# Kernel optimization log

Hardware: AMD Instinct MI355X
Metric: run time of the kernel (lower is better)

The kernel has to match this reference:

```python
import jax, jax.numpy as jnp
import numpy as np

DIM = 768
HID = 1536
EPS = 1e-12
SCALE = float(np.sqrt(DIM))


def _layernorm(x, gamma, beta):
    mu = jnp.mean(x, axis=-1, keepdims=True)
    var = jnp.mean(jnp.square(x - mu), axis=-1, keepdims=True)
    return (x - mu) * jax.lax.rsqrt(var + EPS) * gamma + beta


def setup_inputs() -> dict:
    key = jax.random.key(0)
    ks = jax.random.split(key, 16)
    s = 1.0 / np.sqrt(DIM)
    sh = 1.0 / np.sqrt(HID)
    x = jax.random.normal(ks[0], (8, 2048, DIM), dtype=jnp.float32)
    return {
        "x": x,
        "Wq": jax.random.uniform(ks[1], (DIM, DIM), jnp.float32, -s, s),
        "bq": jax.random.uniform(ks[2], (DIM,), jnp.float32, -s, s),
        "Wk": jax.random.uniform(ks[3], (DIM, DIM), jnp.float32, -s, s),
        "bk": jax.random.uniform(ks[4], (DIM,), jnp.float32, -s, s),
        "Wv": jax.random.uniform(ks[5], (DIM, DIM), jnp.float32, -s, s),
        "bv": jax.random.uniform(ks[6], (DIM,), jnp.float32, -s, s),
        "Wp": jax.random.uniform(ks[7], (DIM, DIM), jnp.float32, -s, s),
        "bp": jax.random.uniform(ks[8], (DIM,), jnp.float32, -s, s),
        "g1": jnp.ones((DIM,), jnp.float32),
        "be1": jnp.zeros((DIM,), jnp.float32),
        "W1": jax.random.uniform(ks[9], (HID, DIM), jnp.float32, -s, s),
        "b1": jax.random.uniform(ks[10], (HID,), jnp.float32, -s, s),
        "W2": jax.random.uniform(ks[11], (DIM, HID), jnp.float32, -sh, sh),
        "b2": jax.random.uniform(ks[12], (DIM,), jnp.float32, -sh, sh),
        "g2": jnp.ones((DIM,), jnp.float32),
        "be2": jnp.zeros((DIM,), jnp.float32),
    }


def reference(x, Wq, bq, Wk, bk, Wv, bv, Wp, bp, g1, be1, W1, b1, W2, b2, g2, be2):
    # NOTE: original code does NOT split into heads; single full-dim bmm attention.
    Q = jnp.einsum("bsd,ed->bse", x, Wq) + bq  # [B,S,D]
    K = jnp.einsum("bsd,ed->bse", x, Wk) + bk
    V = jnp.einsum("bsd,ed->bse", x, Wv) + bv
    alpha = jnp.einsum("bqd,bkd->bqk", Q, K) / SCALE  # [B,S,S]
    alpha = jax.nn.softmax(alpha, axis=-1)
    attn = jnp.einsum("bqk,bkd->bqd", alpha, V)
    attn = jnp.einsum("bsd,ed->bse", attn, Wp) + bp  # linear_proj
    h = _layernorm(x + attn, g1, be1)
    mlp = jax.nn.gelu(jnp.einsum("bsd,hd->bsh", h, W1) + b1, approximate=False)
    mlp = jnp.einsum("bsh,dh->bsd", mlp, W2) + b2
    return _layernorm(h + mlp, g2, be2)
```

## Files before the change

### kernel.cpp

```cpp
#include <hip/hip_runtime.h>
#include <math.h>

#define D_MODEL 768
#define D_HID   1536
#define N_BATCH 8
#define SEQLEN  2048
#define NROWS   (N_BATCH*SEQLEN)

typedef unsigned short u16;
typedef unsigned char  u8;
typedef __attribute__((ext_vector_type(8))) short bfrag;
typedef __attribute__((ext_vector_type(4))) float facc;

__device__ __forceinline__ u16 f2bf(float f) {
  unsigned u = __float_as_uint(f);
  u += 0x7fffu + ((u >> 16) & 1u);
  return (u16)(u >> 16);
}
__device__ __forceinline__ float bf2f(u16 u) {
  return __uint_as_float((unsigned)u << 16);
}
__device__ __forceinline__ u8 f2fp8(float f) {
  return (u8)(__builtin_amdgcn_cvt_pk_fp8_f32(f, f, 0, 0) & 0xff);
}

__device__ __forceinline__ void async16(const void* g, void* l) {
  __builtin_amdgcn_global_load_lds((const __attribute__((address_space(1))) void*)g,
                                   (__attribute__((address_space(3))) void*)l,
                                   16, 0, 0);
}
__device__ __forceinline__ void wg_barrier() {
  asm volatile("" ::: "memory");
  __builtin_amdgcn_s_barrier();
  asm volatile("" ::: "memory");
}
#define VMCNT(n) asm volatile("s_waitcnt vmcnt(" #n ")" ::: "memory")

__global__ __launch_bounds__(256) void cvt_all(
    const float* __restrict__ x,  const float* __restrict__ Wq,
    const float* __restrict__ Wk, const float* __restrict__ Wv,
    const float* __restrict__ Wp, const float* __restrict__ W1,
    const float* __restrict__ W2, const float* __restrict__ bq,
    const float* __restrict__ bk, const float* __restrict__ bv,
    u16* __restrict__ XB, u16* __restrict__ WQKV, u16* __restrict__ WPB,
    u16* __restrict__ W1B, u16* __restrict__ W2B, float* __restrict__ BQKV,
    float* __restrict__ LSUM) {
  long i = (long)blockIdx.x * 256 + threadIdx.x;
  const float* src; u16* dst; long off;
  if      (i < 3145728) { src = x;  dst = XB;             off = i; }
  else if (i < 3293184) { src = Wq; dst = WQKV;           off = i - 3145728; }
  else if (i < 3440640) { src = Wk; dst = WQKV + 589824;  off = i - 3293184; }
  else if (i < 3588096) { src = Wv; dst = WQKV + 1179648; off = i - 3440640; }
  else if (i < 3735552) { src = Wp; dst = WPB;            off = i - 3588096; }
  else if (i < 4030464) { src = W1; dst = W1B;            off = i - 3735552; }
  else if (i < 4325376) { src = W2; dst = W2B;            off = i - 4030464; }
  else if (i < 4325952) {
    long j = i - 4325376;
    const float* s = (j < 192) ? bq : (j < 384) ? bk : bv;
    long o = (j < 192) ? j : (j < 384) ? j - 192 : j - 384;
    ((float4*)BQKV)[j] = ((const float4*)s)[o];
    return;
  } else if (i < 4330048) {
    float4 zz = {0.f, 0.f, 0.f, 0.f};
    ((float4*)LSUM)[i - 4325952] = zz;
    return;
  } else return;
  float4 v = ((const float4*)src)[off];
  ushort4 o4;
  o4.x = f2bf(v.x); o4.y = f2bf(v.y); o4.z = f2bf(v.z); o4.w = f2bf(v.w);
  *reinterpret_cast<ushort4*>(dst + off * 4) = o4;
}

enum { EPI_EXP = 1, EPI_DIV = 2, EPI_GELU = 4, EPI_QKV = 5, EPI_RES = 6 };

template<int EPI>
__global__ __launch_bounds__(512, 4)
void gemm_bt(const u16* __restrict__ Aall, const u16* __restrict__ Ball,
             void* __restrict__ Cout,
             int M, int N, int K,
             long sA, long sB, long sC,
             const float* __restrict__ bias,
             const u16* __restrict__ resid,
             float* __restrict__ lsum,
             float scale)
{
  __shared__ __align__(16) char smem[73728];
  const int z = blockIdx.z;
  const u16* A = Aall + (long)z * sA;
  const u16* B = Ball + (long)z * sB;
  const int bm = blockIdx.x, bn = blockIdx.y;
  const int tid = (int)threadIdx.x;
  const int lane = tid & 63, wv = tid >> 6;
  const int wr = wv >> 2, wc = wv & 3;

  facc acc[4][4] = {};

  const int srow = tid >> 2;
  const int sc = (((tid & 3) ^ (srow & 3)) << 3);
  const u16* Abase = A + (long)(bm * 128) * K;
  const u16* Bbase = B + (long)(bn * 256) * K;
  const int fr = lane & 15, g0 = lane >> 4;
  const int nt = K >> 5;

  auto STAGE = [&](int t, int b) {
    char* Asb = smem + b * 24576;
    char* Bsb = Asb + 8192;
    const long k0 = (long)t << 5;
    async16(Abase + (long)srow * K + k0 + sc, Asb + tid * 16);
    async16(Bbase + (long)srow * K + k0 + sc, Bsb + tid * 16);
    async16(Bbase + (long)(128 + srow) * K + k0 + sc, Bsb + 8192 + tid * 16);
  };

  STAGE(0, 0); STAGE(1, 1);
  int rb_ = 0, sb_ = 2;
  for (int t = 0; t < nt; ++t) {
    if (t < nt - 1) { VMCNT(3); } else { VMCNT(0); }
    wg_barrier();
    if (t + 2 < nt) STAGE(t + 2, sb_);
    const u16* As = (const u16*)(smem + rb_ * 24576);
    const u16* Bs = As + 4096;
    bfrag af[4], bf[4];
#pragma unroll
    for (int i = 0; i < 4; ++i) {
      const int r = wr * 64 + i * 16 + fr;
      af[i] = *(const bfrag*)(As + r * 32 + ((g0 ^ (r & 3)) << 3));
    }
#pragma unroll
    for (int j = 0; j < 4; ++j) {
      const int r = wc * 64 + j * 16 + fr;
      bf[j] = *(const bfrag*)(Bs + r * 32 + ((g0 ^ (r & 3)) << 3));
    }
    __builtin_amdgcn_s_setprio(1);
#pragma unroll
    for (int i = 0; i < 4; ++i)
#pragma unroll
      for (int j = 0; j < 4; ++j)
        acc[i][j] = __builtin_amdgcn_mfma_f32_16x16x32_bf16(af[i], bf[j], acc[i][j], 0, 0, 0);
    __builtin_amdgcn_s_setprio(0);
    rb_ = (rb_ == 2) ? 0 : rb_ + 1;
    sb_ = (sb_ == 2) ? 0 : sb_ + 1;
  }
  wg_barrier();

  const int rb = bm * 128 + wr * 64;
  const int cb = bn * 256 + wc * 64;
  const int quad = lane >> 4;

  if constexpr (EPI == EPI_QKV) {
    const int c64 = bn * 4 + wc;
    const int which = c64 / 12;
    float bj[4];
#pragma unroll
    for (int j = 0; j < 4; ++j) bj[j] = bias[cb + j * 16 + fr];
    if (which == 2) {
      u8* VT_ = (u8*)resid;
      const int zb = rb >> 11;
      const int seqb = (rb & 2047) + quad * 4;
      const int dimb = (c64 - 24) * 64;
#pragma unroll
      for (int i = 0; i < 4; ++i) {
#pragma unroll
        for (int j = 0; j < 4; ++j) {
          const int dim = dimb + j * 16 + fr;
          unsigned v01 = __builtin_amdgcn_cvt_pk_fp8_f32(acc[i][j][0] + bj[j],
                                                         acc[i][j][1] + bj[j], 0, 0);
          unsigned v23 = __builtin_amdgcn_cvt_pk_fp8_f32(acc[i][j][2] + bj[j],
                                                         acc[i][j][3] + bj[j], 0, 0);
          unsigned w = (v01 & 0xffffu) | (v23 << 16);
          *reinterpret_cast<unsigned*>(VT_ + (long)zb * D_MODEL * SEQLEN +
                                       (long)dim * SEQLEN + seqb + i * 16) = w;
        }
      }
      return;
    }
    u8* ep8 = (u8*)(smem + wv * 8192);
    u8* Cg = (u8*)Cout + (long)which * NROWS * D_MODEL;
    const int cbo = (c64 - which * 12) * 64;
#pragma unroll
    for (int i = 0; i < 4; ++i)
#pragma unroll
      for (int r = 0; r < 4; ++r) {
        const int lrow = i * 16 + quad * 4 + r;
#pragma unroll
        for (int j = 0; j < 4; ++j)
          ep8[lrow * 64 + j * 16 + fr] = f2fp8(acc[i][j][r] + bj[j]);
      }
#pragma unroll
    for (int it = 0; it < 4; ++it) {
      const int lr = it * 16 + (lane >> 2);
      const int ch = (lane & 3) << 4;
      int4 d = *(const int4*)(ep8 + lr * 64 + ch);
      *reinterpret_cast<int4*>(Cg + (long)(rb + lr) * D_MODEL + cbo + ch) = d;
    }
  } else {
    u16* ep16 = (u16*)(smem + wv * 8192);
    u16* Cg = (u16*)Cout + (long)z * sC;
    float bj[4];
#pragma unroll
    for (int j = 0; j < 4; ++j) bj[j] = bias[cb + j * 16 + fr];
#pragma unroll
    for (int i = 0; i < 4; ++i) {
#pragma unroll
      for (int r = 0; r < 4; ++r) {
        const int lrow = i * 16 + quad * 4 + r;
#pragma unroll
        for (int j = 0; j < 4; ++j) {
          float t = acc[i][j][r] + bj[j];
          float y = 0.7978845608f * (t + 0.044715f * t * t * t);
          float e = __expf(-2.f * fabsf(y));
          float th = (1.f - e) / (1.f + e);
          th = (y < 0.f) ? -th : th;
          ep16[lrow * 64 + j * 16 + fr] = f2bf(0.5f * t * (1.f + th));
        }
      }
    }
#pragma unroll
    for (int it = 0; it < 8; ++it) {
      const int lr = it * 8 + (lane >> 3);
      const int ch = (lane & 7) << 3;
      int4 d = *(const int4*)(ep16 + lr * 64 + ch);
      *reinterpret_cast<int4*>(Cg + (long)(rb + lr) * N + cb + ch) = d;
    }
  }
}

template<int EPI>
__global__ __launch_bounds__(512, 4)
void gemm_f8(const u8* __restrict__ Aall, const u8* __restrict__ Ball,
             void* __restrict__ Cout,
             int M, int N, int K,
             long sA, long sB, long sC,
             float* __restrict__ lsum, float scale)
{
  __shared__ __align__(16) char smem[73728];
  const int z = blockIdx.z;
  const u8* A = Aall + (long)z * sA;
  const u8* B = Ball + (long)z * sB;
  const int bm = blockIdx.x, bn = blockIdx.y;
  const int tid = (int)threadIdx.x;
  const int lane = tid & 63, wv = tid >> 6;
  const int wr = wv >> 2, wc = wv & 3;

  facc acc[4][4] = {};

  const int srow = tid >> 2;
  const int scb = (((tid & 3) ^ (srow & 3)) << 4);
  const u8* Abase = A + (long)(bm * 128) * K;
  const u8* Bbase = B + (long)(bn * 256) * K;
  const int fr = lane & 15, g0 = lane >> 4;
  const int nt = K >> 6;

  auto STAGE = [&](int t, int b) {
    char* Asb = smem + b * 24576;
    char* Bsb = Asb + 8192;
    const long k0 = (long)t << 6;
    async16(Abase + (long)srow * K + k0 + scb, Asb + tid * 16);
    async16(Bbase + (long)srow * K + k0 + scb, Bsb + tid * 16);
    async16(Bbase + (long)(128 + srow) * K + k0 + scb, Bsb + 8192 + tid * 16);
  };

  STAGE(0, 0); STAGE(1, 1);
  int rb_ = 0, sb_ = 2;
  for (int t = 0; t < nt; ++t) {
    if (t < nt - 1) { VMCNT(3); } else { VMCNT(0); }
    wg_barrier();
    if (t + 2 < nt) STAGE(t + 2, sb_);
    const u8* As = (const u8*)(smem + rb_ * 24576);
    const u8* Bs = As + 8192;
#pragma unroll
    for (int s = 0; s < 2; ++s) {
      long af[4], bf[4];
      const int c = s * 2 + (g0 >> 1);
      const int h8 = (g0 & 1) << 3;
#pragma unroll
      for (int i = 0; i < 4; ++i) {
        const int r = wr * 64 + i * 16 + fr;
        af[i] = *(const long*)(As + r * 64 + ((c ^ (r & 3)) << 4) + h8);
      }
#pragma unroll
      for (int j = 0; j < 4; ++j) {
        const int r = wc * 64 + j * 16 + fr;
        bf[j] = *(const long*)(Bs + r * 64 + ((c ^ (r & 3)) << 4) + h8);
      }
      __builtin_amdgcn_s_setprio(1);
#pragma unroll
      for (int i = 0; i < 4; ++i)
#pragma unroll
        for (int j = 0; j < 4; ++j)
          acc[i][j] = __builtin_amdgcn_mfma_f32_16x16x32_fp8_fp8(af[i], bf[j], acc[i][j], 0, 0, 0);
      __builtin_amdgcn_s_setprio(0);
    }
    rb_ = (rb_ == 2) ? 0 : rb_ + 1;
    sb_ = (sb_ == 2) ? 0 : sb_ + 1;
  }
  wg_barrier();

  const int rb = bm * 128 + wr * 64;
  const int cb = bn * 256 + wc * 64;
  const int quad = lane >> 4;

  if constexpr (EPI == EPI_EXP) {
    u8* ep8 = (u8*)(smem + wv * 4096);
    u8* Cg = (u8*)Cout + (long)z * sC;
#pragma unroll
    for (int i = 0; i < 4; ++i) {
#pragma unroll
      for (int r = 0; r < 4; ++r) {
        const int lrow = i * 16 + quad * 4 + r;
        const int row = rb + lrow;
        float rs = 0.f;
#pragma unroll
        for (int j = 0; j < 4; ++j) {
          float e = __expf(acc[i][j][r] * scale - 3.0f);
          rs += e;
          ep8[lrow * 64 + j * 16 + fr] = f2fp8(e);
        }
        rs += __shfl_xor(rs, 1);
        rs += __shfl_xor(rs, 2);
        rs += __shfl_xor(rs, 4);
        rs += __shfl_xor(rs, 8);
        if (fr == 0) atomicAdd(&lsum[(long)z * M + row], rs);
      }
    }
#pragma unroll
    for (int it = 0; it < 4; ++it) {
      const int lr = it * 16 + (lane >> 2);
      const int ch = (lane & 3) << 4;
      int4 d = *(const int4*)(ep8 + lr * 64 + ch);
      *reinterpret_cast<int4*>(Cg + (long)(rb + lr) * N + cb + ch) = d;
    }
  } else {
    u16* ep16 = (u16*)(smem + wv * 4096);
    u16* Cg = (u16*)Cout + (long)z * sC;
#pragma unroll
    for (int h = 0; h < 2; ++h) {
#pragma unroll
      for (int i2 = 0; i2 < 2; ++i2) {
        const int i = h * 2 + i2;
#pragma unroll
        for (int r = 0; r < 4; ++r) {
          const int lrow = i2 * 16 + quad * 4 + r;
          const int row = rb + h * 32 + lrow;
          const float inv = 1.f / lsum[(long)z * M + row];
#pragma unroll
          for (int j = 0; j < 4; ++j)
            ep16[lrow * 64 + j * 16 + fr] = f2bf(acc[i][j][r] * inv);
        }
      }
#pragma unroll
      for (int it = 0; it < 4; ++it) {
        const int lr = it * 8 + (lane >> 3);
        const int ch = (lane & 7) << 3;
        int4 d = *(const int4*)(ep16 + lr * 64 + ch);
        *reinterpret_cast<int4*>(Cg + (long)(rb + h * 32 + lr) * N + cb + ch) = d;
      }
    }
  }
}

template<int EPI>
__global__ __launch_bounds__(256, 4)
void gemm_bt128(const u16* __restrict__ Aall, const u16* __restrict__ Ball,
                void* __restrict__ Cout,
                int M, int N, int K,
                long sA, long sB, long sC,
                const float* __restrict__ bias,
                const u16* __restrict__ resid,
                float* __restrict__ lsum,
                float scale)
{
  __shared__ __align__(16) char smem[49152];
  const int z = blockIdx.z;
  const u16* A = Aall + (long)z * sA;
  const u16* B = Ball + (long)z * sB;
  const int bm = blockIdx.x, bn = blockIdx.y;
  const int tid = (int)threadIdx.x;
  const int lane = tid & 63, wv = tid >> 6;
  const int wr = wv >> 1, wc = wv & 1;

  facc acc[4][4] = {};

  const int srow = tid >> 2;
  const int sc = (((tid & 3) ^ (srow & 3)) << 3);
  const u16* Abase = A + (long)(bm * 128) * K;
  const u16* Bbase = B + (long)(bn * 128) * K;
  const int fr = lane & 15, g0 = lane >> 4;
  const int nt = K >> 5;

  auto STAGE = [&](int t, int b) {
    char* Asb = smem + b * 16384;
    char* Bsb = Asb + 8192;
    const long k0 = (long)t << 5;
#pragma unroll
    for (int p = 0; p < 2; ++p) {
      async16(Abase + (long)(p * 64 + srow) * K + k0 + sc, Asb + p * 4096 + tid * 16);
      async16(Bbase + (long)(p * 64 + srow) * K + k0 + sc, Bsb + p * 4096 + tid * 16);
    }
  };

  STAGE(0, 0); STAGE(1, 1);
  int rb_ = 0, sb_ = 2;
  for (int t = 0; t < nt; ++t) {
    if (t < nt - 1) { VMCNT(4); } else { VMCNT(0); }
    wg_barrier();
    if (t + 2 < nt) STAGE(t + 2, sb_);
    const u16* As = (const u16*)(smem + rb_ * 16384);
    const u16* Bs = As + 4096;
    bfrag af[4], bf[4];
#pragma unroll
    for (int i = 0; i < 4; ++i) {
      const int r = wr * 64 + i * 16 + fr;
      af[i] = *(const bfrag*)(As + r * 32 + ((g0 ^ (r & 3)) << 3));
    }
#pragma unroll
    for (int j = 0; j < 4; ++j) {
      const int r = wc * 64 + j * 16 + fr;
      bf[j] = *(const bfrag*)(Bs + r * 32 + ((g0 ^ (r & 3)) << 3));
    }
    __builtin_amdgcn_s_setprio(1);
#pragma unroll
    for (int i = 0; i < 4; ++i)
#pragma unroll
      for (int j = 0; j < 4; ++j)
        acc[i][j] = __builtin_amdgcn_mfma_f32_16x16x32_bf16(af[i], bf[j], acc[i][j], 0, 0, 0);
    __builtin_amdgcn_s_setprio(0);
    rb_ = (rb_ == 2) ? 0 : rb_ + 1;
    sb_ = (sb_ == 2) ? 0 : sb_ + 1;
  }
  wg_barrier();

  const int rb = bm * 128 + wr * 64;
  const int cb = bn * 128 + wc * 64;
  const int quad = lane >> 4;

  float* ep32 = (float*)(smem + wv * 8192);
  u16* Cg = (u16*)Cout;
#pragma unroll
  for (int h = 0; h < 2; ++h) {
#pragma unroll
    for (int i2 = 0; i2 < 2; ++i2) {
      const int i = h * 2 + i2;
#pragma unroll
      for (int r = 0; r < 4; ++r) {
        const int lrow = i2 * 16 + quad * 4 + r;
#pragma unroll
        for (int j = 0; j < 4; ++j)
          ep32[lrow * 64 + j * 16 + fr] = acc[i][j][r];
      }
    }
#pragma unroll
    for (int it = 0; it < 8; ++it) {
      const int lr = it * 4 + (lane >> 4);
      const int ch = (lane & 15) << 2;
      float4 d = *(const float4*)(ep32 + lr * 64 + ch);
      const int row = rb + h * 32 + lr;
      const int gcol = cb + ch;
      const long gi = (long)row * N + gcol;
      ushort4 rv = *(const ushort4*)(resid + gi);
      float4 bb = *(const float4*)(bias + gcol);
      ushort4 o;
      o.x = f2bf(d.x + bb.x + bf2f(rv.x));
      o.y = f2bf(d.y + bb.y + bf2f(rv.y));
      o.z = f2bf(d.z + bb.z + bf2f(rv.z));
      o.w = f2bf(d.w + bb.w + bf2f(rv.w));
      *reinterpret_cast<ushort4*>(Cg + gi) = o;
    }
  }
  (void)lsum; (void)scale; (void)sC; (void)M;
}

__global__ __launch_bounds__(192) void layernorm_rows(const u16* __restrict__ in,
                                                      const float* __restrict__ gamma,
                                                      const float* __restrict__ beta,
                                                      float* __restrict__ outf,
                                                      u16* __restrict__ outb) {
  const int row = blockIdx.x;
  const int t = threadIdx.x;
  ushort4 uv = ((const ushort4*)(in + (long)row * D_MODEL))[t];
  float v0 = bf2f(uv.x), v1 = bf2f(uv.y), v2 = bf2f(uv.z), v3 = bf2f(uv.w);
  float s1 = v0 + v1 + v2 + v3;
  float s2 = v0 * v0 + v1 * v1 + v2 * v2 + v3 * v3;
#pragma unroll
  for (int o = 32; o; o >>= 1) { s1 += __shfl_xor(s1, o); s2 += __shfl_xor(s2, o); }
  __shared__ float r1[3], r2[3];
  const int wv = t >> 6, ln = t & 63;
  if (ln == 0) { r1[wv] = s1; r2[wv] = s2; }
  __syncthreads();
  s1 = r1[0] + r1[1] + r1[2];
  s2 = r2[0] + r2[1] + r2[2];
  const float mu = s1 * (1.f / 768.f);
  const float var = s2 * (1.f / 768.f) - mu * mu;
  const float rstd = rsqrtf(var + 1e-12f);
  float4 gv = ((const float4*)gamma)[t];
  float4 bv = ((const float4*)beta)[t];
  float o0 = (v0 - mu) * rstd * gv.x + bv.x;
  float o1 = (v1 - mu) * rstd * gv.y + bv.y;
  float o2 = (v2 - mu) * rstd * gv.z + bv.z;
  float o3 = (v3 - mu) * rstd * gv.w + bv.w;
  if (outf) {
    float4 ov = {o0, o1, o2, o3};
    ((float4*)(outf + (long)row * D_MODEL))[t] = ov;
  }
  if (outb) {
    ushort4 ob;
    ob.x = f2bf(o0); ob.y = f2bf(o1); ob.z = f2bf(o2); ob.w = f2bf(o3);
    ((ushort4*)(outb + (long)row * D_MODEL))[t] = ob;
  }
}

static const size_t OFF_WP   = 0;
static const size_t OFF_W1   = 1179648;
static const size_t OFF_W2   = 3538944;
static const size_t OFF_LSUM = 5898240;
static const size_t OFF_BQKV = 5963776;
static const size_t OFF_QB   = 6291456;
static const size_t OFF_KB   = 18874368;
static const size_t OFF_VT   = 31457280;
static const size_t OFF_EB   = 44040192;
static const size_t OFF_CTX  = 77594624;
static const size_t OFF_XB   = 102760448;
static const size_t OFF_WQKV = 127926272;
static const size_t OFF_M1B  = 131465216;

extern "C" void kernel_launch(void* const* d_in, const int* in_sizes, int n_in,
                              void* d_out, int out_size, void* d_ws, size_t ws_size,
                              hipStream_t stream) {
  const float* x   = (const float*)d_in[0];
  const float* Wq  = (const float*)d_in[1];
  const float* bq  = (const float*)d_in[2];
  const float* Wk  = (const float*)d_in[3];
  const float* bk  = (const float*)d_in[4];
  const float* Wv  = (const float*)d_in[5];
  const float* bv  = (const float*)d_in[6];
  const float* Wp  = (const float*)d_in[7];
  const float* bp  = (const float*)d_in[8];
  const float* g1  = (const float*)d_in[9];
  const float* be1 = (const float*)d_in[10];
  const float* W1  = (const float*)d_in[11];
  const float* b1  = (const float*)d_in[12];
  const float* W2  = (const float*)d_in[13];
  const float* b2  = (const float*)d_in[14];
  const float* g2  = (const float*)d_in[15];
  const float* be2 = (const float*)d_in[16];

  char* ws = (char*)d_ws;
  u16*   WPB  = (u16*)(ws + OFF_WP);
  u16*   W1B  = (u16*)(ws + OFF_W1);
  u16*   W2B  = (u16*)(ws + OFF_W2);
  float* LSUM = (float*)(ws + OFF_LSUM);
  float* BQKV = (float*)(ws + OFF_BQKV);
  u8*    QB   = (u8*)(ws + OFF_QB);
  u8*    KB   = (u8*)(ws + OFF_KB);
  u8*    VT   = (u8*)(ws + OFF_VT);
  u8*    EB   = (u8*)(ws + OFF_EB);
  u16*   CTX  = (u16*)(ws + OFF_CTX);
  u16*   XB   = (u16*)(ws + OFF_XB);
  u16*   WQKV = (u16*)(ws + OFF_WQKV);
  u16*   M1B  = (u16*)(ws + OFF_M1B);
  u16*   PB   = (u16*)(ws + OFF_QB);
  u16*   HB   = (u16*)(ws + OFF_EB);
  u16*   M2B  = (u16*)(ws + OFF_CTX);

  dim3 blk(256), blkg(512), blkl(192);

  cvt_all<<<dim3(16915), blk, 0, stream>>>(x, Wq, Wk, Wv, Wp, W1, W2, bq, bk, bv,
                                           XB, WQKV, WPB, W1B, W2B, BQKV, LSUM);

  gemm_bt<EPI_QKV><<<dim3(128, 9, 1), blkg, 0, stream>>>(XB, WQKV, QB,
      NROWS, 3 * D_MODEL, D_MODEL, 0, 0, 0, BQKV, (const u16*)VT, nullptr, 0.f);

  const float sc = 1.0f / sqrtf((float)D_MODEL);
  gemm_f8<EPI_EXP><<<dim3(16, 8, 8), blkg, 0, stream>>>(QB, KB, EB,
      SEQLEN, SEQLEN, D_MODEL,
      (long)SEQLEN * D_MODEL, (long)SEQLEN * D_MODEL, (long)SEQLEN * SEQLEN,
      LSUM, sc);
  gemm_f8<EPI_DIV><<<dim3(16, 3, 8), blkg, 0, stream>>>(EB, VT, CTX,
      SEQLEN, D_MODEL, SEQLEN,
      (long)SEQLEN * SEQLEN, (long)D_MODEL * SEQLEN, (long)SEQLEN * D_MODEL,
      LSUM, 0.f);
  gemm_bt128<EPI_RES><<<dim3(128, 6, 1), blk, 0, stream>>>(CTX, WPB, PB,
      NROWS, D_MODEL, D_MODEL, 0, 0, 0, bp, XB, nullptr, 0.f);
  layernorm_rows<<<dim3(NROWS), blkl, 0, stream>>>(PB, g1, be1, nullptr, HB);
  gemm_bt<EPI_GELU><<<dim3(128, 6, 1), blkg, 0, stream>>>(HB, W1B, M1B,
      NROWS, D_HID, D_MODEL, 0, 0, 0, b1, nullptr, nullptr, 0.f);
  gemm_bt128<EPI_RES><<<dim3(128, 6, 1), blk, 0, stream>>>(M1B, W2B, M2B,
      NROWS, D_MODEL, D_HID, 0, 0, 0, b2, HB, nullptr, 0.f);
  layernorm_rows<<<dim3(NROWS), blkl, 0, stream>>>(M2B, g2, be2, (float*)d_out, nullptr);

  (void)in_sizes; (void)n_in; (void)out_size; (void)ws_size;
}
```

Baseline: 513.0 us.

## Switch all GEMMs to 128x128 tiles with 256 threads and new LDS swizzle

Converts gemm_bt and gemm_f8 from 128x256 tiles with 8 waves to 128x128 tiles with 4 waves and 48KB LDS, doubling grid sizes along N. It merges gemm_bt128 into gemm_bt as the EPI_RES path. The LDS XOR swizzle key changes from (row&3) to ((row>>1)&3), which is meant to reduce bank conflicts on fragment reads. Smaller tiles mean more blocks and possibly better occupancy, at the cost of lower operand reuse per block and more global traffic for the attention GEMMs.

```diff
diff --git a/kernel.cpp b/kernel.cpp
--- a/kernel.cpp
+++ b/kernel.cpp
@@ -74,7 +74,7 @@
 enum { EPI_EXP = 1, EPI_DIV = 2, EPI_GELU = 4, EPI_QKV = 5, EPI_RES = 6 };
 
 template<int EPI>
-__global__ __launch_bounds__(512, 4)
+__global__ __launch_bounds__(256, 3)
 void gemm_bt(const u16* __restrict__ Aall, const u16* __restrict__ Ball,
              void* __restrict__ Cout,
              int M, int N, int K,
@@ -84,51 +84,56 @@
              float* __restrict__ lsum,
              float scale)
 {
-  __shared__ __align__(16) char smem[73728];
+  __shared__ __align__(16) char smem[49152];
   const int z = blockIdx.z;
   const u16* A = Aall + (long)z * sA;
   const u16* B = Ball + (long)z * sB;
   const int bm = blockIdx.x, bn = blockIdx.y;
   const int tid = (int)threadIdx.x;
   const int lane = tid & 63, wv = tid >> 6;
-  const int wr = wv >> 2, wc = wv & 3;
+  const int wr = wv >> 1, wc = wv & 1;
 
   facc acc[4][4] = {};
 
-  const int srow = tid >> 2;
-  const int sc = (((tid & 3) ^ (srow & 3)) << 3);
+  const int srow2 = tid >> 2;
+  const int c4 = tid & 3;
+  const int skey = (srow2 >> 1) & 3;
+  const int sc = ((c4 ^ skey) << 3);
   const u16* Abase = A + (long)(bm * 128) * K;
-  const u16* Bbase = B + (long)(bn * 256) * K;
+  const u16* Bbase = B + (long)(bn * 128) * K;
   const int fr = lane & 15, g0 = lane >> 4;
+  const int rkey = (fr >> 1) & 3;
   const int nt = K >> 5;
 
   auto STAGE = [&](int t, int b) {
-    char* Asb = smem + b * 24576;
+    char* Asb = smem + b * 16384;
     char* Bsb = Asb + 8192;
     const long k0 = (long)t << 5;
-    async16(Abase + (long)srow * K + k0 + sc, Asb + tid * 16);
-    async16(Bbase + (long)srow * K + k0 + sc, Bsb + tid * 16);
-    async16(Bbase + (long)(128 + srow) * K + k0 + sc, Bsb + 8192 + tid * 16);
+#pragma unroll
+    for (int p = 0; p < 2; ++p) {
+      async16(Abase + (long)(p * 64 + srow2) * K + k0 + sc, Asb + p * 4096 + tid * 16);
+      async16(Bbase + (long)(p * 64 + srow2) * K + k0 + sc, Bsb + p * 4096 + tid * 16);
+    }
   };
 
   STAGE(0, 0); STAGE(1, 1);
   int rb_ = 0, sb_ = 2;
   for (int t = 0; t < nt; ++t) {
-    if (t < nt - 1) { VMCNT(3); } else { VMCNT(0); }
+    if (t < nt - 1) { VMCNT(4); } else { VMCNT(0); }
     wg_barrier();
     if (t + 2 < nt) STAGE(t + 2, sb_);
-    const u16* As = (const u16*)(smem + rb_ * 24576);
+    const u16* As = (const u16*)(smem + rb_ * 16384);
     const u16* Bs = As + 4096;
     bfrag af[4], bf[4];
 #pragma unroll
     for (int i = 0; i < 4; ++i) {
       const int r = wr * 64 + i * 16 + fr;
-      af[i] = *(const bfrag*)(As + r * 32 + ((g0 ^ (r & 3)) << 3));
+      af[i] = *(const bfrag*)(As + r * 32 + ((g0 ^ rkey) << 3));
     }
 #pragma unroll
     for (int j = 0; j < 4; ++j) {
       const int r = wc * 64 + j * 16 + fr;
-      bf[j] = *(const bfrag*)(Bs + r * 32 + ((g0 ^ (r & 3)) << 3));
+      bf[j] = *(const bfrag*)(Bs + r * 32 + ((g0 ^ rkey) << 3));
     }
     __builtin_amdgcn_s_setprio(1);
 #pragma unroll
@@ -143,11 +148,11 @@
   wg_barrier();
 
   const int rb = bm * 128 + wr * 64;
-  const int cb = bn * 256 + wc * 64;
+  const int cb = bn * 128 + wc * 64;
   const int quad = lane >> 4;
 
   if constexpr (EPI == EPI_QKV) {
-    const int c64 = bn * 4 + wc;
+    const int c64 = bn * 2 + wc;
     const int which = c64 / 12;
     float bj[4];
 #pragma unroll
@@ -192,7 +197,7 @@
       int4 d = *(const int4*)(ep8 + lr * 64 + ch);
       *reinterpret_cast<int4*>(Cg + (long)(rb + lr) * D_MODEL + cbo + ch) = d;
     }
-  } else {
+  } else if constexpr (EPI == EPI_GELU) {
     u16* ep16 = (u16*)(smem + wv * 8192);
     u16* Cg = (u16*)Cout + (long)z * sC;
     float bj[4];
@@ -221,66 +226,107 @@
       int4 d = *(const int4*)(ep16 + lr * 64 + ch);
       *reinterpret_cast<int4*>(Cg + (long)(rb + lr) * N + cb + ch) = d;
     }
+  } else {
+    float* ep32 = (float*)(smem + wv * 8192);
+    u16* Cg = (u16*)Cout;
+#pragma unroll
+    for (int h = 0; h < 2; ++h) {
+#pragma unroll
+      for (int i2 = 0; i2 < 2; ++i2) {
+        const int i = h * 2 + i2;
+#pragma unroll
+        for (int r = 0; r < 4; ++r) {
+          const int lrow = i2 * 16 + quad * 4 + r;
+#pragma unroll
+          for (int j = 0; j < 4; ++j)
+            ep32[lrow * 64 + j * 16 + fr] = acc[i][j][r];
+        }
+      }
+#pragma unroll
+      for (int it = 0; it < 8; ++it) {
+        const int lr = it * 4 + (lane >> 4);
+        const int ch = (lane & 15) << 2;
+        float4 d = *(const float4*)(ep32 + lr * 64 + ch);
+        const int row = rb + h * 32 + lr;
+        const int gcol = cb + ch;
+        const long gi = (long)row * N + gcol;
+        ushort4 rv = *(const ushort4*)(resid + gi);
+        float4 bb = *(const float4*)(bias + gcol);
+        ushort4 o;
+        o.x = f2bf(d.x + bb.x + bf2f(rv.x));
+        o.y = f2bf(d.y + bb.y + bf2f(rv.y));
+        o.z = f2bf(d.z + bb.z + bf2f(rv.z));
+        o.w = f2bf(d.w + bb.w + bf2f(rv.w));
+        *reinterpret_cast<ushort4*>(Cg + gi) = o;
+      }
+      wg_barrier();
+    }
   }
+  (void)lsum; (void)scale; (void)M;
 }
 
 template<int EPI>
-__global__ __launch_bounds__(512, 4)
+__global__ __launch_bounds__(256, 3)
 void gemm_f8(const u8* __restrict__ Aall, const u8* __restrict__ Ball,
              void* __restrict__ Cout,
              int M, int N, int K,
              long sA, long sB, long sC,
              float* __restrict__ lsum, float scale)
 {
-  __shared__ __align__(16) char smem[73728];
+  __shared__ __align__(16) char smem[49152];
   const int z = blockIdx.z;
   const u8* A = Aall + (long)z * sA;
   const u8* B = Ball + (long)z * sB;
   const int bm = blockIdx.x, bn = blockIdx.y;
   const int tid = (int)threadIdx.x;
   const int lane = tid & 63, wv = tid >> 6;
-  const int wr = wv >> 2, wc = wv & 3;
+  const int wr = wv >> 1, wc = wv & 1;
 
   facc acc[4][4] = {};
 
-  const int srow = tid >> 2;
-  const int scb = (((tid & 3) ^ (srow & 3)) << 4);
+  const int srow2 = tid >> 2;
+  const int c4 = tid & 3;
+  const int skey = (srow2 >> 1) & 3;
+  const int scb = ((c4 ^ skey) << 4);
   const u8* Abase = A + (long)(bm * 128) * K;
-  const u8* Bbase = B + (long)(bn * 256) * K;
+  const u8* Bbase = B + (long)(bn * 128) * K;
   const int fr = lane & 15, g0 = lane >> 4;
+  const int rkey = (fr >> 1) & 3;
   const int nt = K >> 6;
 
   auto STAGE = [&](int t, int b) {
-    char* Asb = smem + b * 24576;
+    char* Asb = smem + b * 16384;
     char* Bsb = Asb + 8192;
     const long k0 = (long)t << 6;
-    async16(Abase + (long)srow * K + k0 + scb, Asb + tid * 16);
-    async16(Bbase + (long)srow * K + k0 + scb, Bsb + tid * 16);
-    async16(Bbase + (long)(128 + srow) * K + k0 + scb, Bsb + 8192 + tid * 16);
+#pragma unroll
+    for (int p = 0; p < 2; ++p) {
+      async16(Abase + (long)(p * 64 + srow2) * K + k0 + scb, Asb + p * 4096 + tid * 16);
+      async16(Bbase + (long)(p * 64 + srow2) * K + k0 + scb, Bsb + p * 4096 + tid * 16);
+    }
   };
 
   STAGE(0, 0); STAGE(1, 1);
   int rb_ = 0, sb_ = 2;
   for (int t = 0; t < nt; ++t) {
-    if (t < nt - 1) { VMCNT(3); } else { VMCNT(0); }
+    if (t < nt - 1) { VMCNT(4); } else { VMCNT(0); }
     wg_barrier();
     if (t + 2 < nt) STAGE(t + 2, sb_);
-    const u8* As = (const u8*)(smem + rb_ * 24576);
+    const u8* As = (const u8*)(smem + rb_ * 16384);
     const u8* Bs = As + 8192;
 #pragma unroll
     for (int s = 0; s < 2; ++s) {
       long af[4], bf[4];
-      const int c = s * 2 + (g0 >> 1);
+      const int cc = (s * 2 + (g0 >> 1)) ^ rkey;
       const int h8 = (g0 & 1) << 3;
 #pragma unroll
       for (int i = 0; i < 4; ++i) {
         const int r = wr * 64 + i * 16 + fr;
-        af[i] = *(const long*)(As + r * 64 + ((c ^ (r & 3)) << 4) + h8);
+        af[i] = *(const long*)(As + r * 64 + (cc << 4) + h8);
       }
 #pragma unroll
       for (int j = 0; j < 4; ++j) {
         const int r = wc * 64 + j * 16 + fr;
-        bf[j] = *(const long*)(Bs + r * 64 + ((c ^ (r & 3)) << 4) + h8);
+        bf[j] = *(const long*)(Bs + r * 64 + (cc << 4) + h8);
       }
       __builtin_amdgcn_s_setprio(1);
 #pragma unroll
@@ -296,7 +342,7 @@
   wg_barrier();
 
   const int rb = bm * 128 + wr * 64;
-  const int cb = bn * 256 + wc * 64;
+  const int cb = bn * 128 + wc * 64;
   const int quad = lane >> 4;
 
   if constexpr (EPI == EPI_EXP) {
@@ -354,119 +400,9 @@
         int4 d = *(const int4*)(ep16 + lr * 64 + ch);
         *reinterpret_cast<int4*>(Cg + (long)(rb + h * 32 + lr) * N + cb + ch) = d;
       }
+      wg_barrier();
     }
   }
-}
-
-template<int EPI>
-__global__ __launch_bounds__(256, 4)
-void gemm_bt128(const u16* __restrict__ Aall, const u16* __restrict__ Ball,
-                void* __restrict__ Cout,
-                int M, int N, int K,
-                long sA, long sB, long sC,
-                const float* __restrict__ bias,
-                const u16* __restrict__ resid,
-                float* __restrict__ lsum,
-                float scale)
-{
-  __shared__ __align__(16) char smem[49152];
-  const int z = blockIdx.z;
-  const u16* A = Aall + (long)z * sA;
-  const u16* B = Ball + (long)z * sB;
-  const int bm = blockIdx.x, bn = blockIdx.y;
-  const int tid = (int)threadIdx.x;
-  const int lane = tid & 63, wv = tid >> 6;
-  const int wr = wv >> 1, wc = wv & 1;
-
-  facc acc[4][4] = {};
-
-  const int srow = tid >> 2;
-  const int sc = (((tid & 3) ^ (srow & 3)) << 3);
-  const u16* Abase = A + (long)(bm * 128) * K;
-  const u16* Bbase = B + (long)(bn * 128) * K;
-  const int fr = lane & 15, g0 = lane >> 4;
-  const int nt = K >> 5;
-
-  auto STAGE = [&](int t, int b) {
-    char* Asb = smem + b * 16384;
-    char* Bsb = Asb + 8192;
-    const long k0 = (long)t << 5;
-#pragma unroll
-    for (int p = 0; p < 2; ++p) {
-      async16(Abase + (long)(p * 64 + srow) * K + k0 + sc, Asb + p * 4096 + tid * 16);
-      async16(Bbase + (long)(p * 64 + srow) * K + k0 + sc, Bsb + p * 4096 + tid * 16);
-    }
-  };
-
-  STAGE(0, 0); STAGE(1, 1);
-  int rb_ = 0, sb_ = 2;
-  for (int t = 0; t < nt; ++t) {
-    if (t < nt - 1) { VMCNT(4); } else { VMCNT(0); }
-    wg_barrier();
-    if (t + 2 < nt) STAGE(t + 2, sb_);
-    const u16* As = (const u16*)(smem + rb_ * 16384);
-    const u16* Bs = As + 4096;
-    bfrag af[4], bf[4];
-#pragma unroll
-    for (int i = 0; i < 4; ++i) {
-      const int r = wr * 64 + i * 16 + fr;
-      af[i] = *(const bfrag*)(As + r * 32 + ((g0 ^ (r & 3)) << 3));
-    }
-#pragma unroll
-    for (int j = 0; j < 4; ++j) {
-      const int r = wc * 64 + j * 16 + fr;
-      bf[j] = *(const bfrag*)(Bs + r * 32 + ((g0 ^ (r & 3)) << 3));
-    }
-    __builtin_amdgcn_s_setprio(1);
-#pragma unroll
-    for (int i = 0; i < 4; ++i)
-#pragma unroll
-      for (int j = 0; j < 4; ++j)
-        acc[i][j] = __builtin_amdgcn_mfma_f32_16x16x32_bf16(af[i], bf[j], acc[i][j], 0, 0, 0);
-    __builtin_amdgcn_s_setprio(0);
-    rb_ = (rb_ == 2) ? 0 : rb_ + 1;
-    sb_ = (sb_ == 2) ? 0 : sb_ + 1;
-  }
-  wg_barrier();
-
-  const int rb = bm * 128 + wr * 64;
-  const int cb = bn * 128 + wc * 64;
-  const int quad = lane >> 4;
-
-  float* ep32 = (float*)(smem + wv * 8192);
-  u16* Cg = (u16*)Cout;
-#pragma unroll
-  for (int h = 0; h < 2; ++h) {
-#pragma unroll
-    for (int i2 = 0; i2 < 2; ++i2) {
-      const int i = h * 2 + i2;
-#pragma unroll
-      for (int r = 0; r < 4; ++r) {
-        const int lrow = i2 * 16 + quad * 4 + r;
-#pragma unroll
-        for (int j = 0; j < 4; ++j)
-          ep32[lrow * 64 + j * 16 + fr] = acc[i][j][r];
-      }
-    }
-#pragma unroll
-    for (int it = 0; it < 8; ++it) {
-      const int lr = it * 4 + (lane >> 4);
-      const int ch = (lane & 15) << 2;
-      float4 d = *(const float4*)(ep32 + lr * 64 + ch);
-      const int row = rb + h * 32 + lr;
-      const int gcol = cb + ch;
-      const long gi = (long)row * N + gcol;
-      ushort4 rv = *(const ushort4*)(resid + gi);
-      float4 bb = *(const float4*)(bias + gcol);
-      ushort4 o;
-      o.x = f2bf(d.x + bb.x + bf2f(rv.x));
-      o.y = f2bf(d.y + bb.y + bf2f(rv.y));
-      o.z = f2bf(d.z + bb.z + bf2f(rv.z));
-      o.w = f2bf(d.w + bb.w + bf2f(rv.w));
-      *reinterpret_cast<ushort4*>(Cg + gi) = o;
-    }
-  }
-  (void)lsum; (void)scale; (void)sC; (void)M;
 }
 
 __global__ __launch_bounds__(192) void layernorm_rows(const u16* __restrict__ in,
@@ -561,29 +497,29 @@
   u16*   HB   = (u16*)(ws + OFF_EB);
   u16*   M2B  = (u16*)(ws + OFF_CTX);
 
-  dim3 blk(256), blkg(512), blkl(192);
+  dim3 blk(256), blkl(192);
 
   cvt_all<<<dim3(16915), blk, 0, stream>>>(x, Wq, Wk, Wv, Wp, W1, W2, bq, bk, bv,
                                            XB, WQKV, WPB, W1B, W2B, BQKV, LSUM);
 
-  gemm_bt<EPI_QKV><<<dim3(128, 9, 1), blkg, 0, stream>>>(XB, WQKV, QB,
+  gemm_bt<EPI_QKV><<<dim3(128, 18, 1), blk, 0, stream>>>(XB, WQKV, QB,
       NROWS, 3 * D_MODEL, D_MODEL, 0, 0, 0, BQKV, (const u16*)VT, nullptr, 0.f);
 
   const float sc = 1.0f / sqrtf((float)D_MODEL);
-  gemm_f8<EPI_EXP><<<dim3(16, 8, 8), blkg, 0, stream>>>(QB, KB, EB,
+  gemm_f8<EPI_EXP><<<dim3(16, 16, 8), blk, 0, stream>>>(QB, KB, EB,
       SEQLEN, SEQLEN, D_MODEL,
       (long)SEQLEN * D_MODEL, (long)SEQLEN * D_MODEL, (long)SEQLEN * SEQLEN,
       LSUM, sc);
-  gemm_f8<EPI_DIV><<<dim3(16, 3, 8), blkg, 0, stream>>>(EB, VT, CTX,
+  gemm_f8<EPI_DIV><<<dim3(16, 6, 8), blk, 0, stream>>>(EB, VT, CTX,
       SEQLEN, D_MODEL, SEQLEN,
       (long)SEQLEN * SEQLEN, (long)D_MODEL * SEQLEN, (long)SEQLEN * D_MODEL,
       LSUM, 0.f);
-  gemm_bt128<EPI_RES><<<dim3(128, 6, 1), blk, 0, stream>>>(CTX, WPB, PB,
+  gemm_bt<EPI_RES><<<dim3(128, 6, 1), blk, 0, stream>>>(CTX, WPB, PB,
       NROWS, D_MODEL, D_MODEL, 0, 0, 0, bp, XB, nullptr, 0.f);
   layernorm_rows<<<dim3(NROWS), blkl, 0, stream>>>(PB, g1, be1, nullptr, HB);
-  gemm_bt<EPI_GELU><<<dim3(128, 6, 1), blkg, 0, stream>>>(HB, W1B, M1B,
+  gemm_bt<EPI_GELU><<<dim3(128, 12, 1), blk, 0, stream>>>(HB, W1B, M1B,
       NROWS, D_HID, D_MODEL, 0, 0, 0, b1, nullptr, nullptr, 0.f);
-  gemm_bt128<EPI_RES><<<dim3(128, 6, 1), blk, 0, stream>>>(M1B, W2B, M2B,
+  gemm_bt<EPI_RES><<<dim3(128, 6, 1), blk, 0, stream>>>(M1B, W2B, M2B,
       NROWS, D_MODEL, D_HID, 0, 0, 0, b2, HB, nullptr, 0.f);
   layernorm_rows<<<dim3(NROWS), blkl, 0, stream>>>(M2B, g2, be2, (float*)d_out, nullptr);
 
```

Measured after the change: 466.7 us. 1.1x faster.
